# Kernel tuning notes

Hardware: AMD Instinct MI355X
Metric: run time of the kernel (lower is better)

## Reference

```python
import jax, jax.numpy as jnp
import numpy as np

B, IN, N, P, M, D = 32, 4096, 2048, 128, 256, 10
TAU_B, TAU_A, BETA = 1.0, 1.0, 1.0
EPS = 1e-12


def setup_inputs() -> dict:
    key = jax.random.key(0)
    k1, k2, k3, k4, k5 = jax.random.split(key, 5)
    x = jax.random.normal(k1, (B, IN), jnp.float32)
    # fixed random synapse connection pairs (Minchinton cells)
    idx_a = jax.random.randint(k2, (N, P), 0, IN, dtype=jnp.int32)
    idx_b = jax.random.randint(k3, (N, P), 0, IN, dtype=jnp.int32)
    # learned memory bank: raw key patterns and output values, per neuron
    keys_raw = jax.random.normal(k4, (N, M, P), jnp.float32)
    values = jax.random.normal(k5, (N, M, D), jnp.float32)
    return {"x": x, "idx_a": idx_a, "idx_b": idx_b, "keys_raw": keys_raw, "values": values}


def reference(x, idx_a, idx_b, keys_raw, values):
    # Minchinton layer: soft bit = sigmoid of difference of two sampled inputs
    bits = jax.nn.sigmoid((x[:, idx_a] - x[:, idx_b]) / TAU_B)   # (B, N, P)
    # memory keys passed through bit-sigmoid
    keys = jax.nn.sigmoid(keys_raw / TAU_A)                      # (N, M, P)
    # Euclidean cdist per neuron via the quadratic expansion (no (B,N,M,P) temp)
    b_sq = jnp.sum(bits * bits, axis=-1)                         # (B, N)
    k_sq = jnp.sum(keys * keys, axis=-1)                         # (N, M)
    dots = jnp.einsum('bnp,nmp->bnm', bits, keys)                # (B, N, M)
    d2 = jnp.maximum(b_sq[:, :, None] + k_sq[None, :, :] - 2.0 * dots, 0.0)
    dist = jnp.sqrt(d2 + EPS)                                    # (B, N, M)
    # softmin over memory entries, then weighted retrieval of stored values
    w = jax.nn.softmax(-BETA * dist, axis=-1)                    # (B, N, M)
    out = jnp.einsum('bnm,nmd->bnd', w, values)                  # (B, N, D)
    return out
```

## Files before the change

### kernel.cpp

```cpp
#include <hip/hip_runtime.h>

#define B_  32
#define IN_ 4096
#define N_  2048
#define P_  128
#define M_  256
#define D_  10

typedef _Float16 f16;
typedef f16  f16x4   __attribute__((ext_vector_type(4)));
typedef f16  f16x8   __attribute__((ext_vector_type(8)));
typedef float f32x4  __attribute__((ext_vector_type(4)));
typedef float floatx4 __attribute__((ext_vector_type(4)));

union F8 { f16x8 v; f16x4 h[2]; };

__device__ __forceinline__ float sigmoidf_(float z) {
    return __builtin_amdgcn_rcpf(1.0f + __expf(-z));
}

__global__ __launch_bounds__(256, 3) void vgram_kernel(
    const float* __restrict__ x, const int* __restrict__ idx_a, const int* __restrict__ idx_b,
    const float* __restrict__ keys_raw, const float* __restrict__ values, float* __restrict__ out)
{
    const int n   = blockIdx.x;
    const int t   = threadIdx.x;
    const int l   = t & 63;
    const int wv  = t >> 6;
    const int lhi = l >> 4;
    const int l15 = l & 15;

    __shared__ __align__(16) int s_ia[P_], s_ib[P_];
    __shared__ __align__(16) f16 s_bits[B_][P_];
    __shared__ __align__(16) f16 s_keys[64][P_];
    __shared__ __align__(16) f16 s_w[B_][M_];
    __shared__ __align__(16) f16 s_val[M_][18];
    __shared__ float s_bsq[B_];
    __shared__ float s_ksq[M_];

    if (t < 128) { s_ia[t] = idx_a[n * P_ + t]; }
    else         { int tt = t - 128; s_ib[tt] = idx_b[n * P_ + tt]; }
    {
        const float* vb = values + (size_t)n * (M_ * D_);
        #pragma unroll
        for (int it = 0; it < 10; ++it) {
            int f = it * 256 + t;
            float vvv = vb[f];
            int m = f / 10, d = f % 10;
            s_val[m][d] = (f16)vvv;
        }
        s_val[t][10] = (f16)1.0f;
        #pragma unroll
        for (int dd = 11; dd < 16; ++dd) s_val[t][dd] = (f16)0.0f;
    }
    __syncthreads();

    #pragma unroll
    for (int it = 0; it < 4; ++it) {
        int sig = it * 256 + t;
        int b = sig >> 5, q = sig & 31;
        const float* xr = x + b * IN_;
        float partial = 0.f;
        f16x4 hh;
        #pragma unroll
        for (int r = 0; r < 4; ++r) {
            int p = q * 4 + r;
            float z = xr[s_ia[p]] - xr[s_ib[p]];
            float s = sigmoidf_(z);
            f16 hs = (f16)s;
            float hf = (float)hs;
            partial += hf * hf;
            hh[r] = hs;
        }
        *(f16x4*)&s_bits[b][((q ^ (b & 15)) << 2)] = hh;
        #pragma unroll
        for (int off = 1; off < 32; off <<= 1)
            partial += __shfl_xor(partial, off, 32);
        if ((t & 31) == 0) s_bsq[b] = partial;
    }
    __syncthreads();

    F8 afrag[2][4];
    #pragma unroll
    for (int rt = 0; rt < 2; ++rt) {
        int b = rt * 16 + l15;
        #pragma unroll
        for (int ks = 0; ks < 4; ++ks) {
            int u1 = (ks * 8 + lhi) ^ l15;
            int u2 = u1 ^ 4;
            afrag[rt][ks].h[0] = *(const f16x4*)&s_bits[b][u1 << 2];
            afrag[rt][ks].h[1] = *(const f16x4*)&s_bits[b][u2 << 2];
        }
    }

    f32x4 acc[4][2] = {};

    const float* kb_base = keys_raw + (size_t)n * (M_ * P_);
    #pragma unroll
    for (int ck = 0; ck < 4; ++ck) {
        const float* kb = kb_base + ck * (64 * P_);
        #pragma unroll
        for (int it = 0; it < 8; ++it) {
            int f = it * 256 + t;
            int m = f >> 5, q = f & 31;
            floatx4 kvv = *(const floatx4*)(kb + f * 4);
            float partial = 0.f;
            f16x4 hh;
            #pragma unroll
            for (int r = 0; r < 4; ++r) {
                float s = sigmoidf_(kvv[r]);
                f16 hs = (f16)s;
                float hf = (float)hs;
                partial += hf * hf;
                hh[r] = hs;
            }
            *(f16x4*)&s_keys[m][((q ^ (m & 15)) << 2)] = hh;
            #pragma unroll
            for (int off = 1; off < 32; off <<= 1)
                partial += __shfl_xor(partial, off, 32);
            if ((t & 31) == 0) s_ksq[ck * 64 + m] = partial;
        }
        __syncthreads();

        int mrow = wv * 16 + l15;
        #pragma unroll
        for (int ks = 0; ks < 4; ++ks) {
            int u1 = (ks * 8 + lhi) ^ l15;
            int u2 = u1 ^ 4;
            F8 bfrag;
            bfrag.h[0] = *(const f16x4*)&s_keys[mrow][u1 << 2];
            bfrag.h[1] = *(const f16x4*)&s_keys[mrow][u2 << 2];
            acc[ck][0] = __builtin_amdgcn_mfma_f32_16x16x32_f16(afrag[0][ks].v, bfrag.v, acc[ck][0], 0, 0, 0);
            acc[ck][1] = __builtin_amdgcn_mfma_f32_16x16x32_f16(afrag[1][ks].v, bfrag.v, acc[ck][1], 0, 0, 0);
        }
        __syncthreads();
    }

    #pragma unroll
    for (int ck = 0; ck < 4; ++ck) {
        int mg = ck * 64 + wv * 16 + l15;
        float ksq = s_ksq[mg];
        #pragma unroll
        for (int rt = 0; rt < 2; ++rt) {
            #pragma unroll
            for (int reg = 0; reg < 4; ++reg) {
                int b = rt * 16 + lhi * 4 + reg;
                float dots = acc[ck][rt][reg];
                float d2 = s_bsq[b] + ksq - 2.f * dots;
                d2 = fmaxf(d2, 0.f) + 1e-12f;
                float dist = sqrtf(d2);
                float wexp = __expf(-dist);
                int u = mg >> 2;
                s_w[b][((u ^ (b & 15)) << 2) | (mg & 3)] = (f16)wexp;
            }
        }
    }
    __syncthreads();

    if (wv == 0) {
        f32x4 c2[2] = {};
        #pragma unroll
        for (int ks2 = 0; ks2 < 8; ++ks2) {
            F8 bfrag;
            #pragma unroll
            for (int e = 0; e < 8; ++e) {
                int mm = ks2 * 32 + (e >> 2) * 16 + lhi * 4 + (e & 3);
                bfrag.h[e >> 2][e & 3] = s_val[mm][l15];
            }
            #pragma unroll
            for (int rt = 0; rt < 2; ++rt) {
                int b = rt * 16 + l15;
                int u1 = (ks2 * 8 + lhi) ^ l15;
                int u2 = u1 ^ 4;
                F8 af;
                af.h[0] = *(const f16x4*)&s_w[b][u1 << 2];
                af.h[1] = *(const f16x4*)&s_w[b][u2 << 2];
                c2[rt] = __builtin_amdgcn_mfma_f32_16x16x32_f16(af.v, bfrag.v, c2[rt], 0, 0, 0);
            }
        }
        #pragma unroll
        for (int rt = 0; rt < 2; ++rt) {
            #pragma unroll
            for (int reg = 0; reg < 4; ++reg) {
                float sum = __shfl(c2[rt][reg], (l & 48) | 10, 64);
                float rs = 1.0f / sum;
                if (l15 < 10) {
                    int b = rt * 16 + lhi * 4 + reg;
                    out[((size_t)b * N_ + n) * D_ + l15] = c2[rt][reg] * rs;
                }
            }
        }
    }
}

extern "C" void kernel_launch(void* const* d_in, const int* in_sizes, int n_in,
                              void* d_out, int out_size, void* d_ws, size_t ws_size,
                              hipStream_t stream) {
    const float* x    = (const float*)d_in[0];
    const int*   ia   = (const int*)d_in[1];
    const int*   ib   = (const int*)d_in[2];
    const float* keys = (const float*)d_in[3];
    const float* vals = (const float*)d_in[4];
    float* o = (float*)d_out;
    vgram_kernel<<<dim3(N_), dim3(256), 0, stream>>>(x, ia, ib, keys, vals, o);
}
```

Baseline: 432.2 us.

## Alias shared buffers, prefetch key chunks into registers, raise occupancy target

Shared memory is packed into one aliased buffer: s_w reuses the s_bits region, and s_val rows shrink from 18 to 12 halves. This cuts per-block LDS so five blocks per CU can fit. The next key chunk is now software-prefetched into registers while the current chunk is converted. Index arrays are read straight from global memory as int4 vectors instead of staged through LDS, and the A fragments are reloaded from LDS on every chunk instead of being held in registers. The changes trade register pressure (the eight float4 prefetch registers against the tighter launch bound) and extra LDS reads for higher occupancy and better latency hiding. Columns 12-15 read past each row's end into the next row, and the padded rows produce output values that are discarded.

```diff
diff --git a/kernel.cpp b/kernel.cpp
--- a/kernel.cpp
+++ b/kernel.cpp
@@ -12,6 +12,7 @@
 typedef f16  f16x8   __attribute__((ext_vector_type(8)));
 typedef float f32x4  __attribute__((ext_vector_type(4)));
 typedef float floatx4 __attribute__((ext_vector_type(4)));
+typedef int   intx4   __attribute__((ext_vector_type(4)));
 
 union F8 { f16x8 v; f16x4 h[2]; };
 
@@ -19,7 +20,7 @@
     return __builtin_amdgcn_rcpf(1.0f + __expf(-z));
 }
 
-__global__ __launch_bounds__(256, 3) void vgram_kernel(
+__global__ __launch_bounds__(256, 5) void vgram_kernel(
     const float* __restrict__ x, const int* __restrict__ idx_a, const int* __restrict__ idx_b,
     const float* __restrict__ keys_raw, const float* __restrict__ values, float* __restrict__ out)
 {
@@ -30,44 +31,48 @@
     const int lhi = l >> 4;
     const int l15 = l & 15;
 
-    __shared__ __align__(16) int s_ia[P_], s_ib[P_];
-    __shared__ __align__(16) f16 s_bits[B_][P_];
-    __shared__ __align__(16) f16 s_keys[64][P_];
-    __shared__ __align__(16) f16 s_w[B_][M_];
-    __shared__ __align__(16) f16 s_val[M_][18];
-    __shared__ float s_bsq[B_];
-    __shared__ float s_ksq[M_];
-
-    if (t < 128) { s_ia[t] = idx_a[n * P_ + t]; }
-    else         { int tt = t - 128; s_ib[tt] = idx_b[n * P_ + tt]; }
+    __shared__ __align__(16) unsigned char smem[31888];
+    f16 (*s_bits)[P_] = (f16 (*)[P_])(smem);
+    f16 (*s_keys)[P_] = (f16 (*)[P_])(smem + 8192);
+    f16 (*s_w)[M_]    = (f16 (*)[M_])(smem);
+    f16  *s_val       = (f16*)(smem + 24576);
+    float *s_bsq      = (float*)(smem + 30736);
+    float *s_ksq      = (float*)(smem + 30864);
+
+    const float* kb_base = keys_raw + (size_t)n * (M_ * P_);
+
+    floatx4 pf[8];
+    #pragma unroll
+    for (int it = 0; it < 8; ++it)
+        pf[it] = *(const floatx4*)(kb_base + (it * 256 + t) * 4);
+
     {
         const float* vb = values + (size_t)n * (M_ * D_);
         #pragma unroll
         for (int it = 0; it < 10; ++it) {
             int f = it * 256 + t;
             float vvv = vb[f];
-            int m = f / 10, d = f % 10;
-            s_val[m][d] = (f16)vvv;
-        }
-        s_val[t][10] = (f16)1.0f;
-        #pragma unroll
-        for (int dd = 11; dd < 16; ++dd) s_val[t][dd] = (f16)0.0f;
-    }
-    __syncthreads();
+            int m = f / 10, d = f - m * 10;
+            s_val[m * 12 + d] = (f16)vvv;
+        }
+        s_val[t * 12 + 10] = (f16)1.0f;
+        s_val[t * 12 + 11] = (f16)0.0f;
+        if (t < 8) s_val[3072 + t] = (f16)0.0f;
+    }
 
     #pragma unroll
     for (int it = 0; it < 4; ++it) {
         int sig = it * 256 + t;
         int b = sig >> 5, q = sig & 31;
+        intx4 ia4 = *(const intx4*)(idx_a + n * P_ + q * 4);
+        intx4 ib4 = *(const intx4*)(idx_b + n * P_ + q * 4);
         const float* xr = x + b * IN_;
         float partial = 0.f;
         f16x4 hh;
         #pragma unroll
         for (int r = 0; r < 4; ++r) {
-            int p = q * 4 + r;
-            float z = xr[s_ia[p]] - xr[s_ib[p]];
-            float s = sigmoidf_(z);
-            f16 hs = (f16)s;
+            float z = xr[ia4[r]] - xr[ib4[r]];
+            f16 hs = (f16)sigmoidf_(z);
             float hf = (float)hs;
             partial += hf * hf;
             hh[r] = hs;
@@ -78,42 +83,26 @@
             partial += __shfl_xor(partial, off, 32);
         if ((t & 31) == 0) s_bsq[b] = partial;
     }
-    __syncthreads();
-
-    F8 afrag[2][4];
-    #pragma unroll
-    for (int rt = 0; rt < 2; ++rt) {
-        int b = rt * 16 + l15;
-        #pragma unroll
-        for (int ks = 0; ks < 4; ++ks) {
-            int u1 = (ks * 8 + lhi) ^ l15;
-            int u2 = u1 ^ 4;
-            afrag[rt][ks].h[0] = *(const f16x4*)&s_bits[b][u1 << 2];
-            afrag[rt][ks].h[1] = *(const f16x4*)&s_bits[b][u2 << 2];
-        }
-    }
 
     f32x4 acc[4][2] = {};
 
-    const float* kb_base = keys_raw + (size_t)n * (M_ * P_);
     #pragma unroll
     for (int ck = 0; ck < 4; ++ck) {
-        const float* kb = kb_base + ck * (64 * P_);
         #pragma unroll
         for (int it = 0; it < 8; ++it) {
             int f = it * 256 + t;
             int m = f >> 5, q = f & 31;
-            floatx4 kvv = *(const floatx4*)(kb + f * 4);
             float partial = 0.f;
             f16x4 hh;
             #pragma unroll
             for (int r = 0; r < 4; ++r) {
-                float s = sigmoidf_(kvv[r]);
-                f16 hs = (f16)s;
+                f16 hs = (f16)sigmoidf_(pf[it][r]);
                 float hf = (float)hs;
                 partial += hf * hf;
                 hh[r] = hs;
             }
+            if (ck < 3)
+                pf[it] = *(const floatx4*)(kb_base + (ck + 1) * (64 * P_) + (it * 256 + t) * 4);
             *(f16x4*)&s_keys[m][((q ^ (m & 15)) << 2)] = hh;
             #pragma unroll
             for (int off = 1; off < 32; off <<= 1)
@@ -122,16 +111,22 @@
         }
         __syncthreads();
 
-        int mrow = wv * 16 + l15;
-        #pragma unroll
-        for (int ks = 0; ks < 4; ++ks) {
-            int u1 = (ks * 8 + lhi) ^ l15;
-            int u2 = u1 ^ 4;
-            F8 bfrag;
-            bfrag.h[0] = *(const f16x4*)&s_keys[mrow][u1 << 2];
-            bfrag.h[1] = *(const f16x4*)&s_keys[mrow][u2 << 2];
-            acc[ck][0] = __builtin_amdgcn_mfma_f32_16x16x32_f16(afrag[0][ks].v, bfrag.v, acc[ck][0], 0, 0, 0);
-            acc[ck][1] = __builtin_amdgcn_mfma_f32_16x16x32_f16(afrag[1][ks].v, bfrag.v, acc[ck][1], 0, 0, 0);
+        {
+            int mrow = wv * 16 + l15;
+            #pragma unroll
+            for (int ks = 0; ks < 4; ++ks) {
+                int u1 = (ks * 8 + lhi) ^ l15;
+                int u2 = u1 ^ 4;
+                F8 bfrag, a0, a1;
+                bfrag.h[0] = *(const f16x4*)&s_keys[mrow][u1 << 2];
+                bfrag.h[1] = *(const f16x4*)&s_keys[mrow][u2 << 2];
+                a0.h[0] = *(const f16x4*)&s_bits[l15][u1 << 2];
+                a0.h[1] = *(const f16x4*)&s_bits[l15][u2 << 2];
+                a1.h[0] = *(const f16x4*)&s_bits[16 + l15][u1 << 2];
+                a1.h[1] = *(const f16x4*)&s_bits[16 + l15][u2 << 2];
+                acc[ck][0] = __builtin_amdgcn_mfma_f32_16x16x32_f16(a0.v, bfrag.v, acc[ck][0], 0, 0, 0);
+                acc[ck][1] = __builtin_amdgcn_mfma_f32_16x16x32_f16(a1.v, bfrag.v, acc[ck][1], 0, 0, 0);
+            }
         }
         __syncthreads();
     }
@@ -165,7 +160,7 @@
             #pragma unroll
             for (int e = 0; e < 8; ++e) {
                 int mm = ks2 * 32 + (e >> 2) * 16 + lhi * 4 + (e & 3);
-                bfrag.h[e >> 2][e & 3] = s_val[mm][l15];
+                bfrag.h[e >> 2][e & 3] = s_val[mm * 12 + l15];
             }
             #pragma unroll
             for (int rt = 0; rt < 2; ++rt) {
```

Measured after the change: 458.6 us. +6.1%, slower.
